# Optimization experiments

Hardware: AMD Instinct MI355X
Metric: run time of the kernel (lower is better)

Reference implementation:

```python
import jax, jax.numpy as jnp
import numpy as np

NW = 4096      # num_words in document
H = 768        # encoder hidden size
NC = 49152     # number of candidate spans
MSW = 30       # max_span_width
E = 20         # span width embedding size
M = 1024       # mlp hidden size
SPAN_EMB = 3 * H + E  # ment_emb='attn' -> start + end + attn term + width emb
NEG = -1e10


def setup_inputs() -> dict:
    key = jax.random.key(0)
    ks = jax.random.split(key, 16)
    s = 0.02
    encoded_doc = jax.random.normal(ks[0], (NW, H), jnp.float32)
    cand_starts = jax.random.randint(ks[1], (NC,), 0, NW - MSW)
    widths = jax.random.randint(ks[2], (NC,), 0, MSW)
    cand_ends = cand_starts + widths  # guaranteed < NW
    return {
        "encoded_doc": encoded_doc,
        "cand_starts": cand_starts,
        "cand_ends": cand_ends,
        "width_emb": jax.random.normal(ks[3], (MSW, E), jnp.float32) * s,
        "width_prior_emb": jax.random.normal(ks[4], (MSW, E), jnp.float32) * s,
        "attn_w": jax.random.normal(ks[5], (H,), jnp.float32) * s,
        "attn_b": jnp.zeros((1,), jnp.float32),
        "mlp1_w": jax.random.normal(ks[6], (SPAN_EMB, M), jnp.float32) * s,
        "mlp1_b": jnp.zeros((M,), jnp.float32),
        "mlp2_w": jax.random.normal(ks[7], (M,), jnp.float32) * s,
        "mlp2_b": jnp.zeros((1,), jnp.float32),
        "wmlp1_w": jax.random.normal(ks[8], (E, M), jnp.float32) * s,
        "wmlp1_b": jnp.zeros((M,), jnp.float32),
        "wmlp2_w": jax.random.normal(ks[9], (M,), jnp.float32) * s,
        "wmlp2_b": jnp.zeros((1,), jnp.float32),
    }


def reference(encoded_doc, cand_starts, cand_ends, width_emb, width_prior_emb,
              attn_w, attn_b, mlp1_w, mlp1_b, mlp2_w, mlp2_b,
              wmlp1_w, wmlp1_b, wmlp2_w, wmlp2_b):
    # span width index (clamped), shared by both width embedding tables
    width_idx = jnp.clip(cand_ends - cand_starts, 0, MSW - 1)

    # --- get_span_embeddings ---
    start_emb = encoded_doc[cand_starts]                 # [NC, H]
    end_emb = encoded_doc[cand_ends]                     # [NC, H]
    w_emb = width_emb[width_idx]                         # [NC, E]

    word_attn = encoded_doc @ attn_w + attn_b[0]         # [NW]
    doc_range = jnp.arange(NW)
    ment_mask = (doc_range[None, :] >= cand_starts[:, None]) & \
                (doc_range[None, :] <= cand_ends[:, None])       # [NC, NW]
    # original: (1 - mask)*-1e10 + word_attn
    scores = jnp.where(ment_mask, 0.0, NEG) + word_attn[None, :]
    mention_word_attn = jax.nn.softmax(scores, axis=1)   # [NC, NW]
    attention_term = mention_word_attn @ encoded_doc     # [NC, H]

    span_emb = jnp.concatenate([start_emb, end_emb, w_emb, attention_term],
                               axis=1)                   # [NC, 3H+E]

    # --- mention_mlp scoring (1 hidden ReLU layer -> scalar) ---
    h = jax.nn.relu(span_emb @ mlp1_w + mlp1_b)          # [NC, M]
    mention_logits = h @ mlp2_w + mlp2_b[0]              # [NC]

    # --- get_mention_width_scores ---
    wp = width_prior_emb[width_idx]                      # [NC, E]
    hw = jax.nn.relu(wp @ wmlp1_w + wmlp1_b)             # [NC, M]
    width_scores = hw @ wmlp2_w + wmlp2_b[0]             # [NC]

    return mention_logits + width_scores
```

## Files before the change

### kernel.cpp

```cpp
#include <hip/hip_runtime.h>
#include <math.h>

#define NW 4096
#define H 768
#define NC 49152
#define MSW 30
#define E 20
#define M 1024
#define CHUNK 64
#define NCH (NW / CHUNK)
#define NKT (H / 64)

typedef short bf16x8 __attribute__((ext_vector_type(8)));
typedef unsigned short u16x8 __attribute__((ext_vector_type(8)));
typedef float f32x4 __attribute__((ext_vector_type(4)));

__device__ __forceinline__ unsigned short f2bf(float x) {
    unsigned u = __float_as_uint(x);
    return (unsigned short)((u + 0x7fff + ((u >> 16) & 1)) >> 16);
}
__device__ __forceinline__ float bf2f(unsigned short b) {
    return __uint_as_float(((unsigned)b) << 16);
}
__device__ __forceinline__ void gload16(const void* g, void* l) {
    __builtin_amdgcn_global_load_lds((const __attribute__((address_space(1))) void*)g,
                                     (__attribute__((address_space(3))) void*)l, 16, 0, 0);
}

__global__ __launch_bounds__(256) void k_doc_prep(const float* __restrict__ doc,
                                                  const float* __restrict__ attn_w,
                                                  const float* __restrict__ attn_b,
                                                  unsigned short* __restrict__ docb,
                                                  float* __restrict__ ewa,
                                                  int* __restrict__ hist) {
    if (blockIdx.x < 16) hist[blockIdx.x * 256 + threadIdx.x] = 0;
    int row = blockIdx.x * 4 + (threadIdx.x >> 6);
    int lane = threadIdx.x & 63;
    const float* r = doc + (size_t)row * H;
    float s = 0.f;
    #pragma unroll
    for (int q = 0; q < 3; ++q) {
        int idx = q * 256 + lane * 4;
        float4 v = *reinterpret_cast<const float4*>(r + idx);
        float4 w = *reinterpret_cast<const float4*>(attn_w + idx);
        s += v.x * w.x + v.y * w.y + v.z * w.z + v.w * w.w;
        ushort4 o;
        o.x = f2bf(v.x); o.y = f2bf(v.y); o.z = f2bf(v.z); o.w = f2bf(v.w);
        *reinterpret_cast<ushort4*>(docb + (size_t)row * H + idx) = o;
    }
    #pragma unroll
    for (int off = 32; off > 0; off >>= 1) s += __shfl_down(s, off);
    if (lane == 0) ewa[row] = expf(s + attn_b[0]);
}

__global__ __launch_bounds__(256) void k_cvt_bt(const float* __restrict__ mlp1_w,
                                                unsigned short* __restrict__ Bt) {
    __shared__ float sh[32][33];
    int k0 = blockIdx.x * 32, m0 = blockIdx.y * 32, part = blockIdx.z;
    int rb = part == 0 ? 0 : (part == 1 ? H : (2 * H + E));
    int tx = threadIdx.x & 31, ty = threadIdx.x >> 5;
    #pragma unroll
    for (int it = 0; it < 4; ++it) {
        int kk = ty + it * 8;
        sh[kk][tx] = mlp1_w[(size_t)(rb + k0 + kk) * M + m0 + tx];
    }
    __syncthreads();
    #pragma unroll
    for (int it = 0; it < 4; ++it) {
        int mm = ty + it * 8;
        Bt[(size_t)(part * M + m0 + mm) * H + k0 + tx] = f2bf(sh[tx][mm]);
    }
}

__global__ __launch_bounds__(256) void k_scans2(const float* __restrict__ ewa,
                                                float* __restrict__ Dpre,
                                                const int* __restrict__ hist,
                                                int* __restrict__ offs) {
    __shared__ float shf[256];
    __shared__ int shi[256];
    int t = threadIdx.x;
    if (blockIdx.x == 0) {
        float v[16];
        float sum = 0.f;
        #pragma unroll
        for (int i = 0; i < 16; ++i) { v[i] = ewa[t * 16 + i]; sum += v[i]; }
        shf[t] = sum;
        __syncthreads();
        for (int off = 1; off < 256; off <<= 1) {
            float x = (t >= off) ? shf[t - off] : 0.f;
            __syncthreads();
            shf[t] += x;
            __syncthreads();
        }
        float run = shf[t] - sum;
        #pragma unroll
        for (int i = 0; i < 16; ++i) { run += v[i]; Dpre[t * 16 + i + 1] = run; }
        if (t == 0) Dpre[0] = 0.f;
    } else {
        int v[16];
        int sum = 0;
        #pragma unroll
        for (int i = 0; i < 16; ++i) { v[i] = hist[t * 16 + i]; sum += v[i]; }
        shi[t] = sum;
        __syncthreads();
        for (int off = 1; off < 256; off <<= 1) {
            int x = (t >= off) ? shi[t - off] : 0;
            __syncthreads();
            shi[t] += x;
            __syncthreads();
        }
        int run = shi[t] - sum;
        #pragma unroll
        for (int i = 0; i < 16; ++i) { offs[t * 16 + i] = run; run += v[i]; }
    }
}

__global__ __launch_bounds__(256) void k_pw_ws(const float* __restrict__ width_emb,
                                               const float* __restrict__ mlp1_w,
                                               const float* __restrict__ mlp1_b,
                                               float* __restrict__ PW,
                                               const float* __restrict__ wp_emb,
                                               const float* __restrict__ w1,
                                               const float* __restrict__ b1,
                                               const float* __restrict__ w2,
                                               const float* __restrict__ b2,
                                               float* __restrict__ wscore) {
    __shared__ float red[256];
    int w = blockIdx.x;
    int y = blockIdx.y;
    int tid = threadIdx.x;
    if (y < 4) {
        int m = y * 256 + tid;
        float acc = mlp1_b[m];
        #pragma unroll
        for (int e = 0; e < E; ++e)
            acc += width_emb[w * E + e] * mlp1_w[(size_t)(2 * H + e) * M + m];
        PW[w * M + m] = acc;
    } else {
        float part = 0.f;
        for (int m = tid; m < M; m += 256) {
            float h = b1[m];
            #pragma unroll
            for (int e = 0; e < E; ++e) h += wp_emb[w * E + e] * w1[e * M + m];
            part += fmaxf(h, 0.f) * w2[m];
        }
        red[tid] = part;
        __syncthreads();
        for (int s = 128; s > 0; s >>= 1) {
            if (tid < s) red[tid] += red[tid + s];
            __syncthreads();
        }
        if (tid == 0) wscore[w] = red[0] + b2[0];
    }
}

__global__ __launch_bounds__(256) void k_hist(const int* __restrict__ starts,
                                              int* __restrict__ hist) {
    atomicAdd(&hist[starts[blockIdx.x * 256 + threadIdx.x]], 1);
}
__global__ __launch_bounds__(256) void k_scatter(const int* __restrict__ starts,
                                                 int* __restrict__ offs,
                                                 int* __restrict__ perm) {
    int c = blockIdx.x * 256 + threadIdx.x;
    int p = atomicAdd(&offs[starts[c]], 1);
    perm[p] = c;
}

__global__ __launch_bounds__(512, 2) void k_proj_mfma(const unsigned short* __restrict__ docb,
                                                      const unsigned short* __restrict__ Bt,
                                                      unsigned short* __restrict__ Pse,
                                                      float* __restrict__ Sbuf) {
    __shared__ unsigned short As[2][16384];
    __shared__ unsigned short Bs[2][12288];
    int tid = threadIdx.x;
    int bid = blockIdx.x;
    int xcd = bid & 7, rr0 = bid >> 3;
    int coltile = (xcd & 1) * 8 + (rr0 & 7);
    int rowtile = (xcd >> 1) * 4 + (rr0 >> 3);
    int col0 = coltile * 192;
    int row0 = rowtile * 256;
    int wv = tid >> 6, lane = tid & 63;
    int wr = wv >> 2, wc = wv & 3;

    f32x4 acc[8][3];
    #pragma unroll
    for (int mi = 0; mi < 8; ++mi)
        #pragma unroll
        for (int ni = 0; ni < 3; ++ni) acc[mi][ni] = (f32x4){0.f, 0.f, 0.f, 0.f};

    #define STAGE(buf, k0)                                                            \
        {                                                                             \
            _Pragma("unroll")                                                         \
            for (int i = 0; i < 4; ++i) {                                             \
                int s = i * 512 + tid;                                                \
                int mg = s >> 7, ks = (s >> 6) & 1, g = (s >> 4) & 3, ri = s & 15;    \
                gload16(docb + (size_t)(row0 + mg * 16 + ri) * H + (k0) + ks * 32 + g * 8, \
                        (char*)As[buf] + s * 16);                                     \
            }                                                                         \
            _Pragma("unroll")                                                         \
            for (int i = 0; i < 3; ++i) {                                             \
                int s = i * 512 + tid;                                                \
                int cg = s >> 7, ks = (s >> 6) & 1, g = (s >> 4) & 3, ci = s & 15;    \
                gload16(Bt + (size_t)(col0 + cg * 16 + ci) * H + (k0) + ks * 32 + g * 8, \
                        (char*)Bs[buf] + s * 16);                                     \
            }                                                                         \
        }

    STAGE(0, 0);
    STAGE(1, 64);
    asm volatile("s_waitcnt vmcnt(7)" ::: "memory");
    __builtin_amdgcn_s_barrier();

    #pragma unroll 1
    for (int t = 0; t < NKT; ++t) {
        int cur = t & 1;
        bf16x8 af[2][8], bfr[2][3];
        #pragma unroll
        for (int ks = 0; ks < 2; ++ks) {
            #pragma unroll
            for (int mi = 0; mi < 8; ++mi)
                af[ks][mi] = *reinterpret_cast<const bf16x8*>(
                    (char*)As[cur] + (wr * 8 + mi) * 2048 + ks * 1024 + lane * 16);
            #pragma unroll
            for (int ni = 0; ni < 3; ++ni)
                bfr[ks][ni] = *reinterpret_cast<const bf16x8*>(
                    (char*)Bs[cur] + (wc * 3 + ni) * 2048 + ks * 1024 + lane * 16);
        }
        __builtin_amdgcn_s_setprio(1);
        #pragma unroll
        for (int ks = 0; ks < 2; ++ks)
            #pragma unroll
            for (int mi = 0; mi < 8; ++mi)
                #pragma unroll
                for (int ni = 0; ni < 3; ++ni)
                    acc[mi][ni] = __builtin_amdgcn_mfma_f32_16x16x32_bf16(
                        af[ks][mi], bfr[ks][ni], acc[mi][ni], 0, 0, 0);
        __builtin_amdgcn_s_setprio(0);
        if (t + 2 < NKT) {
            asm volatile("s_waitcnt lgkmcnt(0)" ::: "memory");
            __builtin_amdgcn_sched_barrier(0);
            __builtin_amdgcn_s_barrier();
            STAGE(cur, (t + 2) * 64);
            asm volatile("s_waitcnt vmcnt(7)" ::: "memory");
            __builtin_amdgcn_s_barrier();
        } else if (t + 2 == NKT) {
            asm volatile("s_waitcnt vmcnt(0)" ::: "memory");
            __builtin_amdgcn_s_barrier();
        }
    }
    #undef STAGE

    int cr = (lane >> 4) * 4;
    int cc = lane & 15;
    #pragma unroll
    for (int mi = 0; mi < 8; ++mi) {
        #pragma unroll
        for (int ni = 0; ni < 3; ++ni) {
            int rrow = row0 + wr * 128 + mi * 16 + cr;
            int cabs = col0 + wc * 48 + ni * 16 + cc;
            int part = cabs >> 10;
            int cm = cabs & 1023;
            if (part < 2) {
                unsigned short* dst = Pse + (size_t)rrow * 2048 + part * 1024 + cm;
                #pragma unroll
                for (int j = 0; j < 4; ++j) dst[(size_t)j * 2048] = f2bf(acc[mi][ni][j]);
            } else {
                float* dst = Sbuf + (size_t)rrow * M + cm;
                #pragma unroll
                for (int j = 0; j < 4; ++j) dst[(size_t)j * M] = acc[mi][ni][j];
            }
        }
    }
}

__global__ __launch_bounds__(256) void k_scan1(const float* __restrict__ Sbuf,
                                               const float* __restrict__ ewa,
                                               float* __restrict__ T) {
    int m = blockIdx.x * 256 + threadIdx.x;
    int c = blockIdx.y;
    __shared__ float ew[CHUNK];
    if (threadIdx.x < CHUNK) ew[threadIdx.x] = ewa[c * CHUNK + threadIdx.x];
    __syncthreads();
    const float* base = Sbuf + (size_t)(c * CHUNK) * M + m;
    float acc = 0.f;
    #pragma unroll 8
    for (int i = 0; i < CHUNK; ++i)
        acc += ew[i] * base[(size_t)i * M];
    T[c * M + m] = acc;
}

__global__ __launch_bounds__(256) void k_scan2(float* __restrict__ T) {
    int m = blockIdx.x * 256 + threadIdx.x;
    float v[NCH];
    #pragma unroll
    for (int c = 0; c < NCH; ++c) v[c] = T[c * M + m];
    float run = 0.f;
    #pragma unroll
    for (int c = 0; c < NCH; ++c) { float t = v[c]; T[c * M + m] = run; run += t; }
}

__global__ __launch_bounds__(256) void k_scan3(float* __restrict__ Sbuf,
                                               const float* __restrict__ ewa,
                                               const float* __restrict__ T) {
    int m = blockIdx.x * 256 + threadIdx.x;
    int c = blockIdx.y;
    __shared__ float ew[CHUNK];
    if (threadIdx.x < CHUNK) ew[threadIdx.x] = ewa[c * CHUNK + threadIdx.x];
    __syncthreads();
    float acc = T[c * M + m];
    float* base = Sbuf + (size_t)(c * CHUNK) * M + m;
    #pragma unroll 4
    for (int i = 0; i < CHUNK; ++i) {
        float* p = base + (size_t)i * M;
        acc += ew[i] * (*p);
        *p = acc;
    }
}

__global__ __launch_bounds__(256) void k_cand(const unsigned short* __restrict__ Pse,
                                              const float* __restrict__ Sbuf,
                                              const float* __restrict__ PW,
                                              const float* __restrict__ Dpre,
                                              const float* __restrict__ wscore,
                                              const int* __restrict__ perm,
                                              const int* __restrict__ starts,
                                              const int* __restrict__ ends,
                                              const float* __restrict__ mlp2_w,
                                              const float* __restrict__ mlp2_b,
                                              float* __restrict__ out) {
    int bid = blockIdx.x;
    int eff = (bid & 7) * (12288 / 8) + (bid >> 3);
    int j = eff * 4 + (threadIdx.x >> 6);
    int lane = threadIdx.x & 63;
    int c = perm[j];
    int s = starts[c], e = ends[c];
    int wi = e - s;
    wi = wi < 0 ? 0 : (wi > MSW - 1 ? MSW - 1 : wi);

    float inv = 1.f / (Dpre[e + 1] - Dpre[s]);

    const unsigned short* ps = Pse + (size_t)s * 2048;
    const unsigned short* pe = Pse + (size_t)e * 2048 + 1024;
    const float* se = Sbuf + (size_t)e * M;
    const float* ss = Sbuf + (size_t)(s > 0 ? s - 1 : 0) * M;
    const float* pw = PW + (size_t)wi * M;
    bool has_s = (s > 0);

    float part = 0.f;
    #pragma unroll
    for (int q = 0; q < 2; ++q) {
        int m = lane * 8 + q * 512;
        u16x8 a8 = *reinterpret_cast<const u16x8*>(ps + m);
        u16x8 b8 = *reinterpret_cast<const u16x8*>(pe + m);
        float4 t0 = *reinterpret_cast<const float4*>(se + m);
        float4 t1 = *reinterpret_cast<const float4*>(se + m + 4);
        float4 u0 = make_float4(0.f, 0.f, 0.f, 0.f), u1 = u0;
        if (has_s) {
            u0 = *reinterpret_cast<const float4*>(ss + m);
            u1 = *reinterpret_cast<const float4*>(ss + m + 4);
        }
        float4 w0 = *reinterpret_cast<const float4*>(pw + m);
        float4 w1 = *reinterpret_cast<const float4*>(pw + m + 4);
        float4 v0 = *reinterpret_cast<const float4*>(mlp2_w + m);
        float4 v1 = *reinterpret_cast<const float4*>(mlp2_w + m + 4);
        float x;
        x = bf2f(a8[0]) + bf2f(b8[0]) + w0.x + (t0.x - u0.x) * inv; part += fmaxf(x, 0.f) * v0.x;
        x = bf2f(a8[1]) + bf2f(b8[1]) + w0.y + (t0.y - u0.y) * inv; part += fmaxf(x, 0.f) * v0.y;
        x = bf2f(a8[2]) + bf2f(b8[2]) + w0.z + (t0.z - u0.z) * inv; part += fmaxf(x, 0.f) * v0.z;
        x = bf2f(a8[3]) + bf2f(b8[3]) + w0.w + (t0.w - u0.w) * inv; part += fmaxf(x, 0.f) * v0.w;
        x = bf2f(a8[4]) + bf2f(b8[4]) + w1.x + (t1.x - u1.x) * inv; part += fmaxf(x, 0.f) * v1.x;
        x = bf2f(a8[5]) + bf2f(b8[5]) + w1.y + (t1.y - u1.y) * inv; part += fmaxf(x, 0.f) * v1.y;
        x = bf2f(a8[6]) + bf2f(b8[6]) + w1.z + (t1.z - u1.z) * inv; part += fmaxf(x, 0.f) * v1.z;
        x = bf2f(a8[7]) + bf2f(b8[7]) + w1.w + (t1.w - u1.w) * inv; part += fmaxf(x, 0.f) * v1.w;
    }
    #pragma unroll
    for (int off = 32; off > 0; off >>= 1) part += __shfl_down(part, off);
    if (lane == 0) out[c] = part + mlp2_b[0] + wscore[wi];
}

extern "C" void kernel_launch(void* const* d_in, const int* in_sizes, int n_in,
                              void* d_out, int out_size, void* d_ws, size_t ws_size,
                              hipStream_t stream) {
    const float* encoded_doc = (const float*)d_in[0];
    const int*   cand_starts = (const int*)d_in[1];
    const int*   cand_ends   = (const int*)d_in[2];
    const float* width_emb   = (const float*)d_in[3];
    const float* width_prior = (const float*)d_in[4];
    const float* attn_w      = (const float*)d_in[5];
    const float* attn_b      = (const float*)d_in[6];
    const float* mlp1_w      = (const float*)d_in[7];
    const float* mlp1_b      = (const float*)d_in[8];
    const float* mlp2_w      = (const float*)d_in[9];
    const float* mlp2_b      = (const float*)d_in[10];
    const float* wmlp1_w     = (const float*)d_in[11];
    const float* wmlp1_b     = (const float*)d_in[12];
    const float* wmlp2_w     = (const float*)d_in[13];
    const float* wmlp2_b     = (const float*)d_in[14];
    float* out = (float*)d_out;

    float* Sbuf   = (float*)d_ws;
    float* T      = Sbuf + (size_t)NW * M;
    float* PW     = T + NCH * M;
    float* ewa    = PW + MSW * M;
    float* Dpre   = ewa + NW;
    float* wscore = Dpre + 4160;
    unsigned short* Pse  = (unsigned short*)(wscore + 64);
    unsigned short* docb = Pse + (size_t)NW * 2048;
    unsigned short* Btb  = docb + (size_t)NW * H;
    int* hist = (int*)(Btb + (size_t)3072 * H);
    int* offs = hist + 4096;
    int* perm = offs + 4096;

    k_doc_prep<<<NW / 4, 256, 0, stream>>>(encoded_doc, attn_w, attn_b, docb, ewa, hist);
    k_cvt_bt<<<dim3(H / 32, M / 32, 3), 256, 0, stream>>>(mlp1_w, Btb);
    k_hist<<<NC / 256, 256, 0, stream>>>(cand_starts, hist);
    k_scans2<<<2, 256, 0, stream>>>(ewa, Dpre, hist, offs);
    k_pw_ws<<<dim3(MSW, 5), 256, 0, stream>>>(width_emb, mlp1_w, mlp1_b, PW,
                                              width_prior, wmlp1_w, wmlp1_b,
                                              wmlp2_w, wmlp2_b, wscore);
    k_scatter<<<NC / 256, 256, 0, stream>>>(cand_starts, offs, perm);
    k_proj_mfma<<<256, 512, 0, stream>>>(docb, Btb, Pse, Sbuf);
    k_scan1<<<dim3(M / 256, NCH), 256, 0, stream>>>(Sbuf, ewa, T);
    k_scan2<<<M / 256, 256, 0, stream>>>(T);
    k_scan3<<<dim3(M / 256, NCH), 256, 0, stream>>>(Sbuf, ewa, T);
    k_cand<<<NC / 4, 256, 0, stream>>>(Pse, Sbuf, PW, Dpre, wscore, perm,
                                       cand_starts, cand_ends, mlp2_w, mlp2_b, out);
}
```

Before: 120.4 us.

## Fuse chunk-sum scan into GEMM epilogue and group candidates by start word

The per-chunk weighted sums that k_scan1 computed by re-reading Sbuf are now produced in the projection GEMM epilogue from accumulator registers, using shuffles to reduce across lanes, and k_scan1 is removed. k_cand now launches one block per start word. Each block stages that word's start projection and prefix row in shared memory once, then loops over its candidates through bucket offsets written by the scan kernel. This aims to save a kernel launch and redundant global reads, at the risk of load imbalance when start buckets differ in size.

```diff
diff --git a/kernel.cpp b/kernel.cpp
--- a/kernel.cpp
+++ b/kernel.cpp
@@ -75,7 +75,8 @@
 __global__ __launch_bounds__(256) void k_scans2(const float* __restrict__ ewa,
                                                 float* __restrict__ Dpre,
                                                 const int* __restrict__ hist,
-                                                int* __restrict__ offs) {
+                                                int* __restrict__ offs,
+                                                int* __restrict__ begs) {
     __shared__ float shf[256];
     __shared__ int shi[256];
     int t = threadIdx.x;
@@ -111,7 +112,12 @@
         }
         int run = shi[t] - sum;
         #pragma unroll
-        for (int i = 0; i < 16; ++i) { offs[t * 16 + i] = run; run += v[i]; }
+        for (int i = 0; i < 16; ++i) {
+            offs[t * 16 + i] = run;
+            begs[t * 16 + i] = run;
+            run += v[i];
+        }
+        if (t == 255) begs[4096] = run;
     }
 }
 
@@ -168,8 +174,10 @@
 
 __global__ __launch_bounds__(512, 2) void k_proj_mfma(const unsigned short* __restrict__ docb,
                                                       const unsigned short* __restrict__ Bt,
+                                                      const float* __restrict__ ewa,
                                                       unsigned short* __restrict__ Pse,
-                                                      float* __restrict__ Sbuf) {
+                                                      float* __restrict__ Sbuf,
+                                                      float* __restrict__ T) {
     __shared__ unsigned short As[2][16384];
     __shared__ unsigned short Bs[2][12288];
     int tid = threadIdx.x;
@@ -271,22 +279,29 @@
             }
         }
     }
-}
-
-__global__ __launch_bounds__(256) void k_scan1(const float* __restrict__ Sbuf,
-                                               const float* __restrict__ ewa,
-                                               float* __restrict__ T) {
-    int m = blockIdx.x * 256 + threadIdx.x;
-    int c = blockIdx.y;
-    __shared__ float ew[CHUNK];
-    if (threadIdx.x < CHUNK) ew[threadIdx.x] = ewa[c * CHUNK + threadIdx.x];
-    __syncthreads();
-    const float* base = Sbuf + (size_t)(c * CHUNK) * M + m;
-    float acc = 0.f;
-    #pragma unroll 8
-    for (int i = 0; i < CHUNK; ++i)
-        acc += ew[i] * base[(size_t)i * M];
-    T[c * M + m] = acc;
+    #pragma unroll
+    for (int half = 0; half < 2; ++half) {
+        int chunk = (row0 >> 6) + wr * 2 + half;
+        #pragma unroll
+        for (int ni = 0; ni < 3; ++ni) {
+            int cabs = col0 + wc * 48 + ni * 16 + cc;
+            if (cabs >= 2048) {
+                float psum = 0.f;
+                #pragma unroll
+                for (int mi4 = 0; mi4 < 4; ++mi4) {
+                    int mi = half * 4 + mi4;
+                    int rbase = row0 + wr * 128 + mi * 16 + cr;
+                    #pragma unroll
+                    for (int j = 0; j < 4; ++j)
+                        psum += ewa[rbase + j] * acc[mi][ni][j];
+                }
+                psum += __shfl_down(psum, 16);
+                psum += __shfl_down(psum, 32);
+                if ((lane >> 4) == 0)
+                    T[(size_t)chunk * M + (cabs - 2048)] = psum;
+            }
+        }
+    }
 }
 
 __global__ __launch_bounds__(256) void k_scan2(float* __restrict__ T) {
@@ -323,59 +338,66 @@
                                               const float* __restrict__ Dpre,
                                               const float* __restrict__ wscore,
                                               const int* __restrict__ perm,
-                                              const int* __restrict__ starts,
+                                              const int* __restrict__ begs,
                                               const int* __restrict__ ends,
                                               const float* __restrict__ mlp2_w,
                                               const float* __restrict__ mlp2_b,
                                               float* __restrict__ out) {
+    __shared__ __align__(16) unsigned short ps_l[1024];
+    __shared__ __align__(16) float ss_l[1024];
     int bid = blockIdx.x;
-    int eff = (bid & 7) * (12288 / 8) + (bid >> 3);
-    int j = eff * 4 + (threadIdx.x >> 6);
-    int lane = threadIdx.x & 63;
-    int c = perm[j];
-    int s = starts[c], e = ends[c];
-    int wi = e - s;
-    wi = wi < 0 ? 0 : (wi > MSW - 1 ? MSW - 1 : wi);
-
-    float inv = 1.f / (Dpre[e + 1] - Dpre[s]);
-
-    const unsigned short* ps = Pse + (size_t)s * 2048;
-    const unsigned short* pe = Pse + (size_t)e * 2048 + 1024;
-    const float* se = Sbuf + (size_t)e * M;
-    const float* ss = Sbuf + (size_t)(s > 0 ? s - 1 : 0) * M;
-    const float* pw = PW + (size_t)wi * M;
-    bool has_s = (s > 0);
-
-    float part = 0.f;
-    #pragma unroll
-    for (int q = 0; q < 2; ++q) {
-        int m = lane * 8 + q * 512;
-        u16x8 a8 = *reinterpret_cast<const u16x8*>(ps + m);
-        u16x8 b8 = *reinterpret_cast<const u16x8*>(pe + m);
-        float4 t0 = *reinterpret_cast<const float4*>(se + m);
-        float4 t1 = *reinterpret_cast<const float4*>(se + m + 4);
-        float4 u0 = make_float4(0.f, 0.f, 0.f, 0.f), u1 = u0;
-        if (has_s) {
-            u0 = *reinterpret_cast<const float4*>(ss + m);
-            u1 = *reinterpret_cast<const float4*>(ss + m + 4);
-        }
-        float4 w0 = *reinterpret_cast<const float4*>(pw + m);
-        float4 w1 = *reinterpret_cast<const float4*>(pw + m + 4);
-        float4 v0 = *reinterpret_cast<const float4*>(mlp2_w + m);
-        float4 v1 = *reinterpret_cast<const float4*>(mlp2_w + m + 4);
-        float x;
-        x = bf2f(a8[0]) + bf2f(b8[0]) + w0.x + (t0.x - u0.x) * inv; part += fmaxf(x, 0.f) * v0.x;
-        x = bf2f(a8[1]) + bf2f(b8[1]) + w0.y + (t0.y - u0.y) * inv; part += fmaxf(x, 0.f) * v0.y;
-        x = bf2f(a8[2]) + bf2f(b8[2]) + w0.z + (t0.z - u0.z) * inv; part += fmaxf(x, 0.f) * v0.z;
-        x = bf2f(a8[3]) + bf2f(b8[3]) + w0.w + (t0.w - u0.w) * inv; part += fmaxf(x, 0.f) * v0.w;
-        x = bf2f(a8[4]) + bf2f(b8[4]) + w1.x + (t1.x - u1.x) * inv; part += fmaxf(x, 0.f) * v1.x;
-        x = bf2f(a8[5]) + bf2f(b8[5]) + w1.y + (t1.y - u1.y) * inv; part += fmaxf(x, 0.f) * v1.y;
-        x = bf2f(a8[6]) + bf2f(b8[6]) + w1.z + (t1.z - u1.z) * inv; part += fmaxf(x, 0.f) * v1.z;
-        x = bf2f(a8[7]) + bf2f(b8[7]) + w1.w + (t1.w - u1.w) * inv; part += fmaxf(x, 0.f) * v1.w;
-    }
-    #pragma unroll
-    for (int off = 32; off > 0; off >>= 1) part += __shfl_down(part, off);
-    if (lane == 0) out[c] = part + mlp2_b[0] + wscore[wi];
+    int s = (bid & 7) * 512 + (bid >> 3);
+    int tid = threadIdx.x;
+    {
+        ushort4 p4 = *reinterpret_cast<const ushort4*>(Pse + (size_t)s * 2048 + tid * 4);
+        *reinterpret_cast<ushort4*>(ps_l + tid * 4) = p4;
+        float4 s4 = (s > 0) ? *reinterpret_cast<const float4*>(Sbuf + (size_t)(s - 1) * M + tid * 4)
+                            : make_float4(0.f, 0.f, 0.f, 0.f);
+        *reinterpret_cast<float4*>(ss_l + tid * 4) = s4;
+    }
+    __syncthreads();
+    int beg = begs[s], end = begs[s + 1];
+    int wv = tid >> 6, lane = tid & 63;
+    float dps = Dpre[s];
+
+    for (int j = beg + wv; j < end; j += 4) {
+        int c = perm[j];
+        int e = ends[c];
+        int wi = e - s;
+        wi = wi > MSW - 1 ? MSW - 1 : wi;
+        float inv = 1.f / (Dpre[e + 1] - dps);
+        const unsigned short* pe = Pse + (size_t)e * 2048 + 1024;
+        const float* se = Sbuf + (size_t)e * M;
+        const float* pw = PW + (size_t)wi * M;
+
+        float part = 0.f;
+        #pragma unroll
+        for (int q = 0; q < 2; ++q) {
+            int m = lane * 8 + q * 512;
+            u16x8 a8 = *reinterpret_cast<const u16x8*>(ps_l + m);
+            u16x8 b8 = *reinterpret_cast<const u16x8*>(pe + m);
+            float4 t0 = *reinterpret_cast<const float4*>(se + m);
+            float4 t1 = *reinterpret_cast<const float4*>(se + m + 4);
+            float4 u0 = *reinterpret_cast<const float4*>(ss_l + m);
+            float4 u1 = *reinterpret_cast<const float4*>(ss_l + m + 4);
+            float4 w0 = *reinterpret_cast<const float4*>(pw + m);
+            float4 w1 = *reinterpret_cast<const float4*>(pw + m + 4);
+            float4 v0 = *reinterpret_cast<const float4*>(mlp2_w + m);
+            float4 v1 = *reinterpret_cast<const float4*>(mlp2_w + m + 4);
+            float x;
+            x = bf2f(a8[0]) + bf2f(b8[0]) + w0.x + (t0.x - u0.x) * inv; part += fmaxf(x, 0.f) * v0.x;
+            x = bf2f(a8[1]) + bf2f(b8[1]) + w0.y + (t0.y - u0.y) * inv; part += fmaxf(x, 0.f) * v0.y;
+            x = bf2f(a8[2]) + bf2f(b8[2]) + w0.z + (t0.z - u0.z) * inv; part += fmaxf(x, 0.f) * v0.z;
+            x = bf2f(a8[3]) + bf2f(b8[3]) + w0.w + (t0.w - u0.w) * inv; part += fmaxf(x, 0.f) * v0.w;
+            x = bf2f(a8[4]) + bf2f(b8[4]) + w1.x + (t1.x - u1.x) * inv; part += fmaxf(x, 0.f) * v1.x;
+            x = bf2f(a8[5]) + bf2f(b8[5]) + w1.y + (t1.y - u1.y) * inv; part += fmaxf(x, 0.f) * v1.y;
+            x = bf2f(a8[6]) + bf2f(b8[6]) + w1.z + (t1.z - u1.z) * inv; part += fmaxf(x, 0.f) * v1.z;
+            x = bf2f(a8[7]) + bf2f(b8[7]) + w1.w + (t1.w - u1.w) * inv; part += fmaxf(x, 0.f) * v1.w;
+        }
+        #pragma unroll
+        for (int off = 32; off > 0; off >>= 1) part += __shfl_down(part, off);
+        if (lane == 0) out[c] = part + mlp2_b[0] + wscore[wi];
+    }
 }
 
 extern "C" void kernel_launch(void* const* d_in, const int* in_sizes, int n_in,
@@ -409,20 +431,20 @@
     unsigned short* Btb  = docb + (size_t)NW * H;
     int* hist = (int*)(Btb + (size_t)3072 * H);
     int* offs = hist + 4096;
-    int* perm = offs + 4096;
+    int* begs = offs + 4096;
+    int* perm = begs + 4112;
 
     k_doc_prep<<<NW / 4, 256, 0, stream>>>(encoded_doc, attn_w, attn_b, docb, ewa, hist);
     k_cvt_bt<<<dim3(H / 32, M / 32, 3), 256, 0, stream>>>(mlp1_w, Btb);
     k_hist<<<NC / 256, 256, 0, stream>>>(cand_starts, hist);
-    k_scans2<<<2, 256, 0, stream>>>(ewa, Dpre, hist, offs);
+    k_scans2<<<2, 256, 0, stream>>>(ewa, Dpre, hist, offs, begs);
     k_pw_ws<<<dim3(MSW, 5), 256, 0, stream>>>(width_emb, mlp1_w, mlp1_b, PW,
                                               width_prior, wmlp1_w, wmlp1_b,
                                               wmlp2_w, wmlp2_b, wscore);
     k_scatter<<<NC / 256, 256, 0, stream>>>(cand_starts, offs, perm);
-    k_proj_mfma<<<256, 512, 0, stream>>>(docb, Btb, Pse, Sbuf);
-    k_scan1<<<dim3(M / 256, NCH), 256, 0, stream>>>(Sbuf, ewa, T);
+    k_proj_mfma<<<256, 512, 0, stream>>>(docb, Btb, ewa, Pse, Sbuf, T);
     k_scan2<<<M / 256, 256, 0, stream>>>(T);
     k_scan3<<<dim3(M / 256, NCH), 256, 0, stream>>>(Sbuf, ewa, T);
-    k_cand<<<NC / 4, 256, 0, stream>>>(Pse, Sbuf, PW, Dpre, wscore, perm,
-                                       cand_starts, cand_ends, mlp2_w, mlp2_b, out);
-}
+    k_cand<<<4096, 256, 0, stream>>>(Pse, Sbuf, PW, Dpre, wscore, perm, begs,
+                                     cand_ends, mlp2_w, mlp2_b, out);
+}
```

Result: faster. 116.2 us (-3.5%).
